# Kernel tuning notes

Measured on AMD Instinct MI355X. Metric: run time of the kernel, lower is better.

The kernel has to match this reference:

```python
import jax, jax.numpy as jnp
import numpy as np

THRESHOLD = 0.5
NEG_POS_RATIO = 3
ALPHA = 10.0


def cxcy_to_xy(c):
    return jnp.concatenate([c[..., :2] - c[..., 2:] / 2, c[..., :2] + c[..., 2:] / 2], axis=-1)


def xy_to_cxcy(xy):
    return jnp.concatenate([(xy[..., :2] + xy[..., 2:]) / 2, xy[..., 2:] - xy[..., :2]], axis=-1)


def encode(cxcy, anc):
    # SSD encoding with variances 0.1 / 0.2 expressed as /10 and *5
    return jnp.concatenate([
        (cxcy[..., :2] - anc[..., :2]) / (anc[..., 2:] / 10.0),
        jnp.log(cxcy[..., 2:] / anc[..., 2:]) * 5.0,
    ], axis=-1)


def jaccard(a, b):
    # a: [N,4] corner boxes, b: [P,4] corner boxes -> [N,P] IoU
    lt = jnp.maximum(a[:, None, :2], b[None, :, :2])
    rb = jnp.minimum(a[:, None, 2:], b[None, :, 2:])
    wh = jnp.clip(rb - lt, 0.0)
    inter = wh[..., 0] * wh[..., 1]
    area_a = (a[:, 2] - a[:, 0]) * (a[:, 3] - a[:, 1])
    area_b = (b[:, 2] - b[:, 0]) * (b[:, 3] - b[:, 1])
    return inter / (area_a[:, None] + area_b[None, :] - inter)


def _match(boxes, labels, corner_anchor, center_anchor):
    # boxes: [N_obj,4] corner, labels: [N_obj]
    n_obj = boxes.shape[0]
    iou = jaccard(boxes, corner_anchor)                 # [N_obj, P]
    obj_idx = jnp.argmax(iou, axis=1)                   # best prior per object
    iou = iou.at[jnp.arange(n_obj), obj_idx].set(1.0)   # force-match best prior
    positive = jnp.any(iou >= THRESHOLD, axis=0)        # [P]
    max_prior_idx = jnp.argmax(iou, axis=0)             # best object per prior
    true_cls = (labels[max_prior_idx] + 1) * positive.astype(jnp.int32)
    true_locs = encode(xy_to_cxcy(boxes[max_prior_idx]), center_anchor)
    return positive, true_cls, true_locs


def setup_inputs() -> dict:
    B, P, C, NOBJ = 32, 24564, 21, 24
    keys = jax.random.split(jax.random.key(0), 7)
    pred_cls = jax.random.normal(keys[0], (B, P, C), dtype=jnp.float32)
    pred_loc = jax.random.normal(keys[1], (B, P, 4), dtype=jnp.float32) * 0.1
    cxy = jax.random.uniform(keys[2], (B, NOBJ, 2), minval=0.2, maxval=0.8)
    wh = jax.random.uniform(keys[3], (B, NOBJ, 2), minval=0.05, maxval=0.3)
    gt_boxes = jnp.clip(jnp.concatenate([cxy - wh / 2, cxy + wh / 2], axis=-1), 0.0, 1.0)
    gt_labels = jax.random.randint(keys[4], (B, NOBJ), 0, C - 1, dtype=jnp.int32)
    a_cxy = jax.random.uniform(keys[5], (P, 2), minval=0.0, maxval=1.0)
    a_wh = jax.random.uniform(keys[6], (P, 2), minval=0.05, maxval=0.4)
    center_anchor = jnp.concatenate([a_cxy, a_wh], axis=-1)
    return {"pred_cls": pred_cls, "pred_loc": pred_loc, "gt_boxes": gt_boxes,
            "gt_labels": gt_labels, "center_anchor": center_anchor}


def reference(pred_cls, pred_loc, gt_boxes, gt_labels, center_anchor):
    B, P, C = pred_cls.shape
    corner_anchor = cxcy_to_xy(center_anchor)
    positive, true_cls, true_locs = jax.vmap(_match, in_axes=(0, 0, None, None))(
        gt_boxes, gt_labels, corner_anchor, center_anchor)

    n_pos = positive.sum(axis=1)                        # [B]
    n_pos_total = n_pos.sum().astype(pred_loc.dtype)

    # localization: L1 mean over positive priors (4 coords each)
    pos_f = positive[..., None].astype(pred_loc.dtype)
    loc_loss = (jnp.abs(pred_loc - true_locs) * pos_f).sum() / (n_pos_total * 4.0)

    # per-element cross entropy [B, P]
    logp = jax.nn.log_softmax(pred_cls, axis=-1)
    ce = -jnp.take_along_axis(logp, true_cls[..., None], axis=-1)[..., 0]

    conf_pos = (ce * positive.astype(ce.dtype)).sum()
    ce_neg = jnp.where(positive, 0.0, ce)
    ce_neg_sorted = jnp.sort(ce_neg, axis=1)[:, ::-1]   # descending
    ranks = jnp.arange(P)[None, :]
    hard_mask = (ranks < (NEG_POS_RATIO * n_pos)[:, None]).astype(ce.dtype)
    conf_neg = (ce_neg_sorted * hard_mask).sum()
    conf_loss = (conf_pos + conf_neg) / n_pos_total

    loc_loss = ALPHA * loc_loss
    total_loss = conf_loss + loc_loss
    return total_loss, (conf_loss, loc_loss)
```

## Files before the change

### kernel.cpp

```cpp
#include <hip/hip_runtime.h>
#include <stdint.h>

#define B 32
#define P 24564
#define NCLS 21
#define NOBJ 24
#define THRESH 0.5f
#define NBKT 2048
#define LCAP 6144
#define BKT_BASE 7232

#define OFF_ACC      0
#define OFF_ARRV     24
#define OFF_NPOS     32
#define HDR_WORDS    40
#define OFF_OBJPART  160
#define OFF_HIST     98464
#define OFF_CENEG    360608

typedef unsigned long long u64;
__device__ __forceinline__ u64 umax64(u64 a, u64 b) { return a > b ? a : b; }

__device__ __forceinline__ int ce_bucket(unsigned bits) {
    int bk = (int)(bits >> 17) - BKT_BASE;
    return bk < 0 ? 0 : (bk > 2047 ? 2047 : bk);
}

__global__ __launch_bounds__(256) void k_objmax(
    const float* __restrict__ gt_boxes, const float* __restrict__ anchor,
    char* __restrict__ ws) {
#pragma clang fp contract(off)
    int b = blockIdx.y;
    int j = blockIdx.x;
    int tid = threadIdx.x;
    unsigned* hist = (unsigned*)(ws + OFF_HIST);
    u64* part = (u64*)(ws + OFF_OBJPART);
    if (tid < 128) hist[(b * 16 + j) * 128 + tid] = 0u;
    if (b == 0 && j == 0 && tid < HDR_WORDS) ((unsigned*)ws)[tid] = 0u;
    __shared__ float4 sbox[NOBJ];
    __shared__ u64 sbest[NOBJ];
    if (tid < NOBJ) {
        const float* g = gt_boxes + (size_t)(b * NOBJ + tid) * 4;
        sbox[tid] = make_float4(g[0], g[1], g[2], g[3]);
        sbest[tid] = 0ull;
    }
    __syncthreads();
    u64 best[NOBJ];
#pragma unroll
    for (int n = 0; n < NOBJ; n++) best[n] = 0ull;
    int pend = min(P, (j + 1) * 1536);
    for (int p = j * 1536 + tid; p < pend; p += 256) {
        float4 a = *(const float4*)(anchor + (size_t)p * 4);
        float ax0 = a.x - a.z * 0.5f, ay0 = a.y - a.w * 0.5f;
        float ax1 = a.x + a.z * 0.5f, ay1 = a.y + a.w * 0.5f;
        float area_a = (ax1 - ax0) * (ay1 - ay0);
        unsigned pk = ~(unsigned)p;
#pragma unroll
        for (int n = 0; n < NOBJ; n++) {
            float4 bx = sbox[n];
            float ltx = fmaxf(bx.x, ax0), lty = fmaxf(bx.y, ay0);
            float rbx = fminf(bx.z, ax1), rby = fminf(bx.w, ay1);
            float w = fmaxf(rbx - ltx, 0.f), h = fmaxf(rby - lty, 0.f);
            float inter = w * h;
            float area_o = (bx.z - bx.x) * (bx.w - bx.y);
            float iou = inter / (area_o + area_a - inter);
            u64 key = ((u64)__float_as_uint(iou) << 32) | pk;
            best[n] = umax64(best[n], key);
        }
    }
#pragma unroll
    for (int n = 0; n < NOBJ; n++) {
        u64 v = best[n];
        for (int off = 32; off > 0; off >>= 1) v = umax64(v, __shfl_down(v, off, 64));
        if ((tid & 63) == 0) atomicMax(&sbest[n], v);
    }
    __syncthreads();
    if (tid < NOBJ) part[((size_t)b * NOBJ + tid) * 16 + j] = sbest[tid];
}

__global__ __launch_bounds__(256, 2) void k_mainB(
    const float* __restrict__ pred_cls, const float* __restrict__ pred_loc,
    const float* __restrict__ gt_boxes, const int* __restrict__ gt_labels,
    const float* __restrict__ anchor, char* __restrict__ ws) {
#pragma clang fp contract(off)
    double* acc = (double*)(ws + OFF_ACC);
    int* n_pos = (int*)(ws + OFF_NPOS);
    const u64* objpart = (const u64*)(ws + OFF_OBJPART);
    unsigned* hist = (unsigned*)(ws + OFF_HIST);
    float* ce_neg = (float*)(ws + OFF_CENEG);

    __shared__ float4 sbox[NOBJ];
    __shared__ int slab[NOBJ];
    __shared__ int sobj[NOBJ];
    __shared__ unsigned shist[NBKT];
    __shared__ float swf[8];
    __shared__ int swi[4];
    const int tid = threadIdx.x;
    const int b = blockIdx.x / 24;
    const int j = blockIdx.x % 24;

    for (int i = tid; i < NBKT; i += 256) shist[i] = 0u;
    if (tid < NOBJ) {
        const float* g = gt_boxes + (size_t)(b * NOBJ + tid) * 4;
        sbox[tid] = make_float4(g[0], g[1], g[2], g[3]);
        slab[tid] = gt_labels[b * NOBJ + tid];
        const u64* pp = objpart + ((size_t)b * NOBJ + tid) * 16;
        u64 m = pp[0];
#pragma unroll
        for (int q = 1; q < 16; q++) m = umax64(m, pp[q]);
        sobj[tid] = (int)(~(unsigned)(m & 0xFFFFFFFFull));
    }
    __syncthreads();

    int p0 = j * 1024 + tid * 4;
    float lsum = 0.f, cpos = 0.f;
    int lnp = 0;
    if (p0 < P) {
        float4 xx[21];
        const float4* xp = (const float4*)(pred_cls + ((size_t)b * P + p0) * NCLS);
#pragma unroll
        for (int k = 0; k < 21; k++) xx[k] = xp[k];
        const float* arr = (const float*)xx;
        float4 anc4[4];
#pragma unroll
        for (int r = 0; r < 4; r++) anc4[r] = ((const float4*)anchor)[p0 + r];
        float4 cev;
        float* cevp = (float*)&cev;
#pragma unroll
        for (int r = 0; r < 4; r++) {
            int p = p0 + r;
            float4 a = anc4[r];
            float ax0 = a.x - a.z * 0.5f, ay0 = a.y - a.w * 0.5f;
            float ax1 = a.x + a.z * 0.5f, ay1 = a.y + a.w * 0.5f;
            float area_a = (ax1 - ax0) * (ay1 - ay0);
            float bv = -1.f;
            int bn = 0;
#pragma unroll
            for (int n = 0; n < NOBJ; n++) {
                float4 bx = sbox[n];
                float ltx = fmaxf(bx.x, ax0), lty = fmaxf(bx.y, ay0);
                float rbx = fminf(bx.z, ax1), rby = fminf(bx.w, ay1);
                float w = fmaxf(rbx - ltx, 0.f), h = fmaxf(rby - lty, 0.f);
                float inter = w * h;
                float area_o = (bx.z - bx.x) * (bx.w - bx.y);
                float iou = inter / (area_o + area_a - inter);
                if (p == sobj[n]) iou = 1.0f;
                if (iou > bv) { bv = iou; bn = n; }
            }
            int pos = (bv >= THRESH) ? 1 : 0;
            int cls = pos ? (slab[bn] + 1) : 0;
            const float* x = arr + r * 21;
            float m = x[0];
#pragma unroll
            for (int q = 1; q < NCLS; q++) m = fmaxf(m, x[q]);
            float s = 0.f;
#pragma unroll
            for (int q = 0; q < NCLS; q++) s += __expf(x[q] - m);
            float xc = x[0];
#pragma unroll
            for (int q = 1; q < NCLS; q++) xc = (cls == q) ? x[q] : xc;
            float ce = m + __logf(s) - xc;
            if (pos) {
                lnp++;
                cpos += ce;
                cevp[r] = 0.f;
                float4 bx = sbox[bn];
                float bcx = (bx.x + bx.z) * 0.5f, bcy = (bx.y + bx.w) * 0.5f;
                float bw = bx.z - bx.x, bh = bx.w - bx.y;
                float t0 = (bcx - a.x) / (a.z / 10.0f);
                float t1 = (bcy - a.y) / (a.w / 10.0f);
                float t2 = __logf(bw / a.z) * 5.0f;
                float t3 = __logf(bh / a.w) * 5.0f;
                float4 pl = *(const float4*)(pred_loc + ((size_t)b * P + p) * 4);
                lsum += fabsf(pl.x - t0) + fabsf(pl.y - t1) + fabsf(pl.z - t2) + fabsf(pl.w - t3);
            } else {
                float cen = fmaxf(ce, 0.f);
                cevp[r] = cen;
                atomicAdd(&shist[ce_bucket(__float_as_uint(cen))], 1u);
            }
        }
        *(float4*)(ce_neg + (size_t)b * P + p0) = cev;
    }
    for (int off = 32; off > 0; off >>= 1) {
        lsum += __shfl_down(lsum, off, 64);
        cpos += __shfl_down(cpos, off, 64);
        lnp  += __shfl_down(lnp, off, 64);
    }
    if ((tid & 63) == 0) { swf[tid >> 6] = lsum; swf[4 + (tid >> 6)] = cpos; swi[tid >> 6] = lnp; }
    __syncthreads();
    if (tid == 0) {
        float ls = swf[0] + swf[1] + swf[2] + swf[3];
        float cs = swf[4] + swf[5] + swf[6] + swf[7];
        int np = swi[0] + swi[1] + swi[2] + swi[3];
        if (np) atomicAdd(&n_pos[b], np);
        atomicAdd(&acc[0], (double)ls);
        atomicAdd(&acc[1], (double)cs);
    }
    for (int i = tid; i < NBKT; i += 256) {
        unsigned c = shist[i];
        if (c) atomicAdd(&hist[b * NBKT + i], c);
    }
}

__device__ __forceinline__ void find_bound(const unsigned* shist, int NB, int K,
                                           int* sscal, unsigned* wsum, int tid) {
    int G = NB >> 8;
    unsigned loc[8];
    unsigned tot = 0;
    for (int g = 0; g < G; g++) { loc[g] = shist[tid * G + g]; tot += loc[g]; }
    unsigned v = tot;
    int lane = tid & 63;
    for (int off = 1; off < 64; off <<= 1) {
        unsigned o = __shfl_down(v, off, 64);
        if (lane + off < 64) v += o;
    }
    if (lane == 0) wsum[tid >> 6] = v;
    __syncthreads();
    unsigned above = 0;
    for (int w = (tid >> 6) + 1; w < 4; w++) above += wsum[w];
    unsigned sfx_excl = above + (v - tot);
    unsigned snext = 0, sloc = 0;
    for (int k = G - 1; k >= 0; k--) {
        sloc = snext + loc[k];
        unsigned sfx_i = sloc + sfx_excl;
        unsigned sfx_n = snext + sfx_excl;
        if (sfx_i >= (unsigned)K && sfx_n < (unsigned)K) {
            sscal[0] = tid * G + k;
            sscal[1] = K - (int)sfx_n;
        }
        snext = sloc;
    }
    if (tid == 0) {
        unsigned total = sloc + sfx_excl;
        if (total < (unsigned)K) {
            sscal[0] = 0;
            sscal[1] = K - (int)((sloc - loc[0]) + sfx_excl);
        }
    }
    __syncthreads();
}

__device__ __forceinline__ void find_bound64(const unsigned* h64, int K, int* sscal, int tid) {
    if (tid < 64) {
        unsigned cnt = h64[tid];
        unsigned v = cnt;
        for (int off = 1; off < 64; off <<= 1) {
            unsigned o = __shfl_down(v, off, 64);
            if (tid + off < 64) v += o;
        }
        unsigned vnext = v - cnt;
        if (v >= (unsigned)K && vnext < (unsigned)K) { sscal[0] = tid; sscal[1] = K - (int)vnext; }
    }
    __syncthreads();
}

__global__ __launch_bounds__(256) void k_sel(
    const float* __restrict__ ce_neg, const unsigned* __restrict__ hist,
    const int* __restrict__ n_pos, double* __restrict__ acc,
    unsigned* __restrict__ arrv, float* __restrict__ out) {
    __shared__ unsigned shist[NBKT];
    __shared__ unsigned slist[LCAP];
    __shared__ int swi[4];
    __shared__ double swd[4];
    __shared__ unsigned wsum[4];
    __shared__ int sscal[4];
    const int b = blockIdx.x;
    const int tid = threadIdx.x;
    const int lane = tid & 63;
    int K = n_pos[b] * 3;
    if (K > P) K = P;
    double s = 0.0;
    if (K > 0) {
        for (int i = tid; i < NBKT; i += 256) shist[i] = hist[b * NBKT + i];
        __syncthreads();
        find_bound(shist, NBKT, K, sscal, wsum, tid);
        int b0 = sscal[0], Kp0 = sscal[1];
        if (tid == 0) sscal[2] = 0;
        __syncthreads();
        const uint4* x4 = (const uint4*)(ce_neg + (size_t)b * P);
        for (int i = tid; i < P / 4; i += 256) {
            uint4 v = x4[i];
            unsigned vv[4] = {v.x, v.y, v.z, v.w};
#pragma unroll
            for (int r = 0; r < 4; r++) {
                int bk = ce_bucket(vv[r]);
                if (bk > b0) s += (double)__uint_as_float(vv[r]);
                else if (bk == b0) {
                    int pos = atomicAdd(&sscal[2], 1);
                    if (pos < LCAP) slist[pos] = vv[r];
                }
            }
        }
        __syncthreads();
        int lcnt = sscal[2];
        if (Kp0 > 0) {
            bool clamped = (b0 == 0) || (b0 == 2047);
            if (lcnt <= LCAP && !clamped) {
                for (int i = tid; i < NBKT; i += 256) shist[i] = 0u;
                __syncthreads();
                for (int i = tid; i < lcnt; i += 256)
                    atomicAdd(&shist[(slist[i] >> 6) & 0x7FFu], 1u);
                __syncthreads();
                find_bound(shist, NBKT, Kp0, sscal, wsum, tid);
                int b1 = sscal[0], Kp1 = sscal[1];
                if (tid < 64) shist[tid] = 0u;
                __syncthreads();
                for (int i = tid; i < lcnt; i += 256) {
                    unsigned v = slist[i];
                    int k1 = (int)((v >> 6) & 0x7FFu);
                    if (k1 > b1) s += (double)__uint_as_float(v);
                    else if (k1 == b1) atomicAdd(&shist[v & 0x3Fu], 1u);
                }
                __syncthreads();
                find_bound64(shist, Kp1, sscal, tid);
                int b2 = sscal[0], R = sscal[1];
                for (int i = tid; i < lcnt; i += 256) {
                    unsigned v = slist[i];
                    if ((int)((v >> 6) & 0x7FFu) == b1 && (int)(v & 0x3Fu) > b2)
                        s += (double)__uint_as_float(v);
                }
                unsigned Tbits = ((unsigned)(b0 + BKT_BASE) << 17) | ((unsigned)b1 << 6) | (unsigned)b2;
                if (tid == 0) s += (double)R * (double)__uint_as_float(Tbits);
            } else if (lcnt <= LCAP) {
                unsigned T = 0;
                for (int bit = 30; bit >= 0; bit--) {
                    unsigned cand = T | (1u << bit);
                    int cc = 0;
                    for (int i = tid; i < lcnt; i += 256) cc += (slist[i] >= cand) ? 1 : 0;
                    for (int off = 32; off > 0; off >>= 1) cc += __shfl_down(cc, off, 64);
                    if (lane == 0) swi[tid >> 6] = cc;
                    __syncthreads();
                    int tot = swi[0] + swi[1] + swi[2] + swi[3];
                    __syncthreads();
                    if (tot >= Kp0) T = cand;
                }
                int cgt = 0;
                for (int i = tid; i < lcnt; i += 256) {
                    unsigned v = slist[i];
                    if (v > T) { cgt++; s += (double)__uint_as_float(v); }
                }
                for (int off = 32; off > 0; off >>= 1) cgt += __shfl_down(cgt, off, 64);
                if (lane == 0) swi[tid >> 6] = cgt;
                __syncthreads();
                if (tid == 0) {
                    int cg = swi[0] + swi[1] + swi[2] + swi[3];
                    s += (double)(Kp0 - cg) * (double)__uint_as_float(T);
                }
                __syncthreads();
            } else {
                const unsigned* src = (const unsigned*)(ce_neg + (size_t)b * P);
                unsigned T = 0;
                for (int bit = 30; bit >= 0; bit--) {
                    unsigned cand = T | (1u << bit);
                    int cc = 0;
                    for (int i = tid; i < P; i += 256) {
                        unsigned v = src[i];
                        if (ce_bucket(v) == b0 && v >= cand) cc++;
                    }
                    for (int off = 32; off > 0; off >>= 1) cc += __shfl_down(cc, off, 64);
                    if (lane == 0) swi[tid >> 6] = cc;
                    __syncthreads();
                    int tot = swi[0] + swi[1] + swi[2] + swi[3];
                    __syncthreads();
                    if (tot >= Kp0) T = cand;
                }
                int cgt = 0;
                for (int i = tid; i < P; i += 256) {
                    unsigned v = src[i];
                    if (ce_bucket(v) == b0 && v > T) { cgt++; s += (double)__uint_as_float(v); }
                }
                for (int off = 32; off > 0; off >>= 1) cgt += __shfl_down(cgt, off, 64);
                if (lane == 0) swi[tid >> 6] = cgt;
                __syncthreads();
                if (tid == 0) {
                    int cg = swi[0] + swi[1] + swi[2] + swi[3];
                    s += (double)(Kp0 - cg) * (double)__uint_as_float(T);
                }
                __syncthreads();
            }
        }
        for (int off = 32; off > 0; off >>= 1) s += __shfl_down(s, off, 64);
        if (lane == 0) swd[tid >> 6] = s;
        __syncthreads();
        if (tid == 0) atomicAdd(&acc[2], swd[0] + swd[1] + swd[2] + swd[3]);
    }
    __syncthreads();
    if (tid == 0) {
        __threadfence();
        unsigned done = __hip_atomic_fetch_add(arrv, 1u, __ATOMIC_ACQ_REL,
                                               __HIP_MEMORY_SCOPE_AGENT);
        if (done == B - 1) {
            int npt = 0;
            for (int k = 0; k < B; k++)
                npt += __hip_atomic_load((int*)&n_pos[k], __ATOMIC_RELAXED,
                                         __HIP_MEMORY_SCOPE_AGENT);
            u64 u0 = __hip_atomic_load((u64*)&acc[0], __ATOMIC_RELAXED, __HIP_MEMORY_SCOPE_AGENT);
            u64 u1 = __hip_atomic_load((u64*)&acc[1], __ATOMIC_RELAXED, __HIP_MEMORY_SCOPE_AGENT);
            u64 u2 = __hip_atomic_load((u64*)&acc[2], __ATOMIC_RELAXED, __HIP_MEMORY_SCOPE_AGENT);
            double a0 = __longlong_as_double((long long)u0);
            double a1 = __longlong_as_double((long long)u1);
            double a2 = __longlong_as_double((long long)u2);
            double npf = (double)npt;
            float conf = (float)((a1 + a2) / npf);
            float loc = 10.0f * (float)(a0 / (npf * 4.0));
            out[0] = conf + loc;
            out[1] = conf;
            out[2] = loc;
        }
    }
}

extern "C" void kernel_launch(void* const* d_in, const int* in_sizes, int n_in,
                              void* d_out, int out_size, void* d_ws, size_t ws_size,
                              hipStream_t stream) {
    const float* pred_cls = (const float*)d_in[0];
    const float* pred_loc = (const float*)d_in[1];
    const float* gt_boxes = (const float*)d_in[2];
    const int*   gt_labels = (const int*)d_in[3];
    const float* anchor   = (const float*)d_in[4];
    float* out = (float*)d_out;
    char* ws = (char*)d_ws;
    double* acc = (double*)(ws + OFF_ACC);
    unsigned* arrv = (unsigned*)(ws + OFF_ARRV);
    int* n_pos = (int*)(ws + OFF_NPOS);
    unsigned* hist = (unsigned*)(ws + OFF_HIST);
    float* ce_neg = (float*)(ws + OFF_CENEG);

    k_objmax<<<dim3(16, B), 256, 0, stream>>>(gt_boxes, anchor, ws);
    k_mainB<<<24 * B, 256, 0, stream>>>(pred_cls, pred_loc, gt_boxes, gt_labels, anchor, ws);
    k_sel<<<B, 256, 0, stream>>>(ce_neg, hist, n_pos, acc, arrv, out);
}
```

Before: 180.2 us.

## Fuse hard-negative selection into main kernel via last-block-per-batch arrival

Merges the per-batch hard-negative selection kernel into the main loss kernel. Each block bumps a per-batch arrival counter, and the 24th block to finish a batch runs the histogram bound search and top-K sum for that batch. A global counter still finalizes the output. This removes one kernel launch and lets selection for early batches overlap with main work on other batches. In exchange it raises shared memory per block with the selection list, which may pressure occupancy, and relies on atomics and fences for cross-block visibility.

```diff
diff --git a/kernel.cpp b/kernel.cpp
--- a/kernel.cpp
+++ b/kernel.cpp
@@ -11,12 +11,13 @@
 #define BKT_BASE 7232
 
 #define OFF_ACC      0
-#define OFF_ARRV     24
-#define OFF_NPOS     32
-#define HDR_WORDS    40
-#define OFF_OBJPART  160
-#define OFF_HIST     98464
-#define OFF_CENEG    360608
+#define OFF_ARRVALL  24
+#define OFF_BARRV    32
+#define OFF_NPOS     160
+#define HDR_WORDS    72
+#define OFF_OBJPART  288
+#define OFF_HIST     98592
+#define OFF_CENEG    360736
 
 typedef unsigned long long u64;
 __device__ __forceinline__ u64 umax64(u64 a, u64 b) { return a > b ? a : b; }
@@ -78,12 +79,66 @@
     if (tid < NOBJ) part[((size_t)b * NOBJ + tid) * 16 + j] = sbest[tid];
 }
 
-__global__ __launch_bounds__(256, 2) void k_mainB(
+__device__ __forceinline__ void find_bound(const unsigned* shist, int NB, int K,
+                                           int* sscal, unsigned* wsum, int tid) {
+    int G = NB >> 8;
+    unsigned loc[8];
+    unsigned tot = 0;
+    for (int g = 0; g < G; g++) { loc[g] = shist[tid * G + g]; tot += loc[g]; }
+    unsigned v = tot;
+    int lane = tid & 63;
+    for (int off = 1; off < 64; off <<= 1) {
+        unsigned o = __shfl_down(v, off, 64);
+        if (lane + off < 64) v += o;
+    }
+    if (lane == 0) wsum[tid >> 6] = v;
+    __syncthreads();
+    unsigned above = 0;
+    for (int w = (tid >> 6) + 1; w < 4; w++) above += wsum[w];
+    unsigned sfx_excl = above + (v - tot);
+    unsigned snext = 0, sloc = 0;
+    for (int k = G - 1; k >= 0; k--) {
+        sloc = snext + loc[k];
+        unsigned sfx_i = sloc + sfx_excl;
+        unsigned sfx_n = snext + sfx_excl;
+        if (sfx_i >= (unsigned)K && sfx_n < (unsigned)K) {
+            sscal[0] = tid * G + k;
+            sscal[1] = K - (int)sfx_n;
+        }
+        snext = sloc;
+    }
+    if (tid == 0) {
+        unsigned total = sloc + sfx_excl;
+        if (total < (unsigned)K) {
+            sscal[0] = 0;
+            sscal[1] = K - (int)((sloc - loc[0]) + sfx_excl);
+        }
+    }
+    __syncthreads();
+}
+
+__device__ __forceinline__ void find_bound64(const unsigned* h64, int K, int* sscal, int tid) {
+    if (tid < 64) {
+        unsigned cnt = h64[tid];
+        unsigned v = cnt;
+        for (int off = 1; off < 64; off <<= 1) {
+            unsigned o = __shfl_down(v, off, 64);
+            if (tid + off < 64) v += o;
+        }
+        unsigned vnext = v - cnt;
+        if (v >= (unsigned)K && vnext < (unsigned)K) { sscal[0] = tid; sscal[1] = K - (int)vnext; }
+    }
+    __syncthreads();
+}
+
+__global__ __launch_bounds__(256, 2) void k_fused(
     const float* __restrict__ pred_cls, const float* __restrict__ pred_loc,
     const float* __restrict__ gt_boxes, const int* __restrict__ gt_labels,
-    const float* __restrict__ anchor, char* __restrict__ ws) {
+    const float* __restrict__ anchor, char* __restrict__ ws, float* __restrict__ out) {
 #pragma clang fp contract(off)
     double* acc = (double*)(ws + OFF_ACC);
+    unsigned* arrv_all = (unsigned*)(ws + OFF_ARRVALL);
+    unsigned* batch_arrv = (unsigned*)(ws + OFF_BARRV);
     int* n_pos = (int*)(ws + OFF_NPOS);
     const u64* objpart = (const u64*)(ws + OFF_OBJPART);
     unsigned* hist = (unsigned*)(ws + OFF_HIST);
@@ -93,9 +148,16 @@
     __shared__ int slab[NOBJ];
     __shared__ int sobj[NOBJ];
     __shared__ unsigned shist[NBKT];
+    __shared__ unsigned slist[LCAP];
     __shared__ float swf[8];
     __shared__ int swi[4];
+    __shared__ double swd[4];
+    __shared__ unsigned wsum[4];
+    __shared__ int sscal[4];
+    __shared__ int swin;
+
     const int tid = threadIdx.x;
+    const int lane = tid & 63;
     const int b = blockIdx.x / 24;
     const int j = blockIdx.x % 24;
 
@@ -186,7 +248,7 @@
         cpos += __shfl_down(cpos, off, 64);
         lnp  += __shfl_down(lnp, off, 64);
     }
-    if ((tid & 63) == 0) { swf[tid >> 6] = lsum; swf[4 + (tid >> 6)] = cpos; swi[tid >> 6] = lnp; }
+    if (lane == 0) { swf[tid >> 6] = lsum; swf[4 + (tid >> 6)] = cpos; swi[tid >> 6] = lnp; }
     __syncthreads();
     if (tid == 0) {
         float ls = swf[0] + swf[1] + swf[2] + swf[3];
@@ -200,78 +262,25 @@
         unsigned c = shist[i];
         if (c) atomicAdd(&hist[b * NBKT + i], c);
     }
-}
-
-__device__ __forceinline__ void find_bound(const unsigned* shist, int NB, int K,
-                                           int* sscal, unsigned* wsum, int tid) {
-    int G = NB >> 8;
-    unsigned loc[8];
-    unsigned tot = 0;
-    for (int g = 0; g < G; g++) { loc[g] = shist[tid * G + g]; tot += loc[g]; }
-    unsigned v = tot;
-    int lane = tid & 63;
-    for (int off = 1; off < 64; off <<= 1) {
-        unsigned o = __shfl_down(v, off, 64);
-        if (lane + off < 64) v += o;
-    }
-    if (lane == 0) wsum[tid >> 6] = v;
-    __syncthreads();
-    unsigned above = 0;
-    for (int w = (tid >> 6) + 1; w < 4; w++) above += wsum[w];
-    unsigned sfx_excl = above + (v - tot);
-    unsigned snext = 0, sloc = 0;
-    for (int k = G - 1; k >= 0; k--) {
-        sloc = snext + loc[k];
-        unsigned sfx_i = sloc + sfx_excl;
-        unsigned sfx_n = snext + sfx_excl;
-        if (sfx_i >= (unsigned)K && sfx_n < (unsigned)K) {
-            sscal[0] = tid * G + k;
-            sscal[1] = K - (int)sfx_n;
-        }
-        snext = sloc;
-    }
+
+    __syncthreads();
     if (tid == 0) {
-        unsigned total = sloc + sfx_excl;
-        if (total < (unsigned)K) {
-            sscal[0] = 0;
-            sscal[1] = K - (int)((sloc - loc[0]) + sfx_excl);
-        }
-    }
-    __syncthreads();
-}
-
-__device__ __forceinline__ void find_bound64(const unsigned* h64, int K, int* sscal, int tid) {
-    if (tid < 64) {
-        unsigned cnt = h64[tid];
-        unsigned v = cnt;
-        for (int off = 1; off < 64; off <<= 1) {
-            unsigned o = __shfl_down(v, off, 64);
-            if (tid + off < 64) v += o;
-        }
-        unsigned vnext = v - cnt;
-        if (v >= (unsigned)K && vnext < (unsigned)K) { sscal[0] = tid; sscal[1] = K - (int)vnext; }
-    }
-    __syncthreads();
-}
-
-__global__ __launch_bounds__(256) void k_sel(
-    const float* __restrict__ ce_neg, const unsigned* __restrict__ hist,
-    const int* __restrict__ n_pos, double* __restrict__ acc,
-    unsigned* __restrict__ arrv, float* __restrict__ out) {
-    __shared__ unsigned shist[NBKT];
-    __shared__ unsigned slist[LCAP];
-    __shared__ int swi[4];
-    __shared__ double swd[4];
-    __shared__ unsigned wsum[4];
-    __shared__ int sscal[4];
-    const int b = blockIdx.x;
-    const int tid = threadIdx.x;
-    const int lane = tid & 63;
-    int K = n_pos[b] * 3;
+        __threadfence();
+        unsigned old = __hip_atomic_fetch_add(&batch_arrv[b], 1u,
+                                              __ATOMIC_ACQ_REL, __HIP_MEMORY_SCOPE_AGENT);
+        swin = (old == 23) ? 1 : 0;
+    }
+    __syncthreads();
+    if (swin == 0) return;
+
+    int npb = __hip_atomic_load(&n_pos[b], __ATOMIC_RELAXED, __HIP_MEMORY_SCOPE_AGENT);
+    int K = npb * 3;
     if (K > P) K = P;
     double s = 0.0;
     if (K > 0) {
-        for (int i = tid; i < NBKT; i += 256) shist[i] = hist[b * NBKT + i];
+        for (int i = tid; i < NBKT; i += 256)
+            shist[i] = __hip_atomic_load(&hist[b * NBKT + i],
+                                         __ATOMIC_RELAXED, __HIP_MEMORY_SCOPE_AGENT);
         __syncthreads();
         find_bound(shist, NBKT, K, sscal, wsum, tid);
         int b0 = sscal[0], Kp0 = sscal[1];
@@ -384,16 +393,16 @@
         __syncthreads();
         if (tid == 0) atomicAdd(&acc[2], swd[0] + swd[1] + swd[2] + swd[3]);
     }
+
     __syncthreads();
     if (tid == 0) {
         __threadfence();
-        unsigned done = __hip_atomic_fetch_add(arrv, 1u, __ATOMIC_ACQ_REL,
-                                               __HIP_MEMORY_SCOPE_AGENT);
-        if (done == B - 1) {
+        unsigned old = __hip_atomic_fetch_add(arrv_all, 1u,
+                                              __ATOMIC_ACQ_REL, __HIP_MEMORY_SCOPE_AGENT);
+        if (old == B - 1) {
             int npt = 0;
             for (int k = 0; k < B; k++)
-                npt += __hip_atomic_load((int*)&n_pos[k], __ATOMIC_RELAXED,
-                                         __HIP_MEMORY_SCOPE_AGENT);
+                npt += __hip_atomic_load(&n_pos[k], __ATOMIC_RELAXED, __HIP_MEMORY_SCOPE_AGENT);
             u64 u0 = __hip_atomic_load((u64*)&acc[0], __ATOMIC_RELAXED, __HIP_MEMORY_SCOPE_AGENT);
             u64 u1 = __hip_atomic_load((u64*)&acc[1], __ATOMIC_RELAXED, __HIP_MEMORY_SCOPE_AGENT);
             u64 u2 = __hip_atomic_load((u64*)&acc[2], __ATOMIC_RELAXED, __HIP_MEMORY_SCOPE_AGENT);
@@ -420,13 +429,8 @@
     const float* anchor   = (const float*)d_in[4];
     float* out = (float*)d_out;
     char* ws = (char*)d_ws;
-    double* acc = (double*)(ws + OFF_ACC);
-    unsigned* arrv = (unsigned*)(ws + OFF_ARRV);
-    int* n_pos = (int*)(ws + OFF_NPOS);
-    unsigned* hist = (unsigned*)(ws + OFF_HIST);
-    float* ce_neg = (float*)(ws + OFF_CENEG);
 
     k_objmax<<<dim3(16, B), 256, 0, stream>>>(gt_boxes, anchor, ws);
-    k_mainB<<<24 * B, 256, 0, stream>>>(pred_cls, pred_loc, gt_boxes, gt_labels, anchor, ws);
-    k_sel<<<B, 256, 0, stream>>>(ce_neg, hist, n_pos, acc, arrv, out);
-}
+    k_fused<<<24 * B, 256, 0, stream>>>(pred_cls, pred_loc, gt_boxes, gt_labels,
+                                        anchor, ws, out);
+}
```

Result: slower. 213.4 us (+18.4%).

## Halve per-thread work in main kernel and widen selection kernel to 1024 threads

Applied to the files above, without the earlier changes.

The main kernel now gives each thread 2 priors instead of 4. That doubles the grid to 48 blocks per image and raises the launch-bounds occupancy hint from 2 to 4, to get more waves in flight and fewer registers per thread. The IoU loop now reads precomputed box areas from shared memory and uses a hardware reciprocal instead of a divide, with fp contraction re-enabled. The selection kernel runs with 1024 threads per block, with a 16-wave block reduction helper and find_bound restricted to the first 256 threads. In exchange it accepts small numeric differences from the approximate reciprocal and FMA contraction, plus more per-block histogram flush atomics.

```diff
diff --git a/kernel.cpp b/kernel.cpp
--- a/kernel.cpp
+++ b/kernel.cpp
@@ -78,11 +78,10 @@
     if (tid < NOBJ) part[((size_t)b * NOBJ + tid) * 16 + j] = sbest[tid];
 }
 
-__global__ __launch_bounds__(256, 2) void k_mainB(
+__global__ __launch_bounds__(256, 4) void k_mainB(
     const float* __restrict__ pred_cls, const float* __restrict__ pred_loc,
     const float* __restrict__ gt_boxes, const int* __restrict__ gt_labels,
     const float* __restrict__ anchor, char* __restrict__ ws) {
-#pragma clang fp contract(off)
     double* acc = (double*)(ws + OFF_ACC);
     int* n_pos = (int*)(ws + OFF_NPOS);
     const u64* objpart = (const u64*)(ws + OFF_OBJPART);
@@ -90,19 +89,21 @@
     float* ce_neg = (float*)(ws + OFF_CENEG);
 
     __shared__ float4 sbox[NOBJ];
+    __shared__ float sarea[NOBJ];
     __shared__ int slab[NOBJ];
     __shared__ int sobj[NOBJ];
     __shared__ unsigned shist[NBKT];
     __shared__ float swf[8];
     __shared__ int swi[4];
     const int tid = threadIdx.x;
-    const int b = blockIdx.x / 24;
-    const int j = blockIdx.x % 24;
+    const int b = blockIdx.x / 48;
+    const int j = blockIdx.x % 48;
 
     for (int i = tid; i < NBKT; i += 256) shist[i] = 0u;
     if (tid < NOBJ) {
         const float* g = gt_boxes + (size_t)(b * NOBJ + tid) * 4;
         sbox[tid] = make_float4(g[0], g[1], g[2], g[3]);
+        sarea[tid] = (g[2] - g[0]) * (g[3] - g[1]);
         slab[tid] = gt_labels[b * NOBJ + tid];
         const u64* pp = objpart + ((size_t)b * NOBJ + tid) * 16;
         u64 m = pp[0];
@@ -112,24 +113,24 @@
     }
     __syncthreads();
 
-    int p0 = j * 1024 + tid * 4;
+    int p0 = j * 512 + tid * 2;
     float lsum = 0.f, cpos = 0.f;
     int lnp = 0;
     if (p0 < P) {
-        float4 xx[21];
-        const float4* xp = (const float4*)(pred_cls + ((size_t)b * P + p0) * NCLS);
+        float2 xx[21];
+        const float2* xp = (const float2*)(pred_cls + ((size_t)b * P + p0) * NCLS);
 #pragma unroll
         for (int k = 0; k < 21; k++) xx[k] = xp[k];
         const float* arr = (const float*)xx;
-        float4 anc4[4];
-#pragma unroll
-        for (int r = 0; r < 4; r++) anc4[r] = ((const float4*)anchor)[p0 + r];
-        float4 cev;
+        float4 anc2[2];
+        anc2[0] = ((const float4*)anchor)[p0];
+        anc2[1] = ((const float4*)anchor)[p0 + 1];
+        float2 cev;
         float* cevp = (float*)&cev;
 #pragma unroll
-        for (int r = 0; r < 4; r++) {
+        for (int r = 0; r < 2; r++) {
             int p = p0 + r;
-            float4 a = anc4[r];
+            float4 a = anc2[r];
             float ax0 = a.x - a.z * 0.5f, ay0 = a.y - a.w * 0.5f;
             float ax1 = a.x + a.z * 0.5f, ay1 = a.y + a.w * 0.5f;
             float area_a = (ax1 - ax0) * (ay1 - ay0);
@@ -142,8 +143,8 @@
                 float rbx = fminf(bx.z, ax1), rby = fminf(bx.w, ay1);
                 float w = fmaxf(rbx - ltx, 0.f), h = fmaxf(rby - lty, 0.f);
                 float inter = w * h;
-                float area_o = (bx.z - bx.x) * (bx.w - bx.y);
-                float iou = inter / (area_o + area_a - inter);
+                float den = sarea[n] + area_a - inter;
+                float iou = inter * __builtin_amdgcn_rcpf(den);
                 if (p == sobj[n]) iou = 1.0f;
                 if (iou > bv) { bv = iou; bn = n; }
             }
@@ -179,7 +180,7 @@
                 atomicAdd(&shist[ce_bucket(__float_as_uint(cen))], 1u);
             }
         }
-        *(float4*)(ce_neg + (size_t)b * P + p0) = cev;
+        *(float2*)(ce_neg + (size_t)b * P + p0) = cev;
     }
     for (int off = 32; off > 0; off >>= 1) {
         lsum += __shfl_down(lsum, off, 64);
@@ -206,35 +207,39 @@
                                            int* sscal, unsigned* wsum, int tid) {
     int G = NB >> 8;
     unsigned loc[8];
-    unsigned tot = 0;
-    for (int g = 0; g < G; g++) { loc[g] = shist[tid * G + g]; tot += loc[g]; }
-    unsigned v = tot;
-    int lane = tid & 63;
-    for (int off = 1; off < 64; off <<= 1) {
-        unsigned o = __shfl_down(v, off, 64);
-        if (lane + off < 64) v += o;
-    }
-    if (lane == 0) wsum[tid >> 6] = v;
-    __syncthreads();
-    unsigned above = 0;
-    for (int w = (tid >> 6) + 1; w < 4; w++) above += wsum[w];
-    unsigned sfx_excl = above + (v - tot);
-    unsigned snext = 0, sloc = 0;
-    for (int k = G - 1; k >= 0; k--) {
-        sloc = snext + loc[k];
-        unsigned sfx_i = sloc + sfx_excl;
-        unsigned sfx_n = snext + sfx_excl;
-        if (sfx_i >= (unsigned)K && sfx_n < (unsigned)K) {
-            sscal[0] = tid * G + k;
-            sscal[1] = K - (int)sfx_n;
-        }
-        snext = sloc;
-    }
-    if (tid == 0) {
-        unsigned total = sloc + sfx_excl;
-        if (total < (unsigned)K) {
-            sscal[0] = 0;
-            sscal[1] = K - (int)((sloc - loc[0]) + sfx_excl);
+    unsigned tot = 0, v = 0;
+    if (tid < 256) {
+        for (int g = 0; g < G; g++) { loc[g] = shist[tid * G + g]; tot += loc[g]; }
+        v = tot;
+        int lane = tid & 63;
+        for (int off = 1; off < 64; off <<= 1) {
+            unsigned o = __shfl_down(v, off, 64);
+            if (lane + off < 64) v += o;
+        }
+        if (lane == 0) wsum[tid >> 6] = v;
+    }
+    __syncthreads();
+    if (tid < 256) {
+        unsigned above = 0;
+        for (int w = (tid >> 6) + 1; w < 4; w++) above += wsum[w];
+        unsigned sfx_excl = above + (v - tot);
+        unsigned snext = 0, sloc = 0;
+        for (int k = G - 1; k >= 0; k--) {
+            sloc = snext + loc[k];
+            unsigned sfx_i = sloc + sfx_excl;
+            unsigned sfx_n = snext + sfx_excl;
+            if (sfx_i >= (unsigned)K && sfx_n < (unsigned)K) {
+                sscal[0] = tid * G + k;
+                sscal[1] = K - (int)sfx_n;
+            }
+            snext = sloc;
+        }
+        if (tid == 0) {
+            unsigned total = sloc + sfx_excl;
+            if (total < (unsigned)K) {
+                sscal[0] = 0;
+                sscal[1] = K - (int)((sloc - loc[0]) + sfx_excl);
+            }
         }
     }
     __syncthreads();
@@ -254,31 +259,41 @@
     __syncthreads();
 }
 
-__global__ __launch_bounds__(256) void k_sel(
+__device__ __forceinline__ int bsum16i(int v, int* buf, int tid) {
+    for (int off = 32; off > 0; off >>= 1) v += __shfl_down(v, off, 64);
+    if ((tid & 63) == 0) buf[tid >> 6] = v;
+    __syncthreads();
+    int r = 0;
+#pragma unroll
+    for (int w = 0; w < 16; w++) r += buf[w];
+    __syncthreads();
+    return r;
+}
+
+__global__ __launch_bounds__(1024) void k_sel(
     const float* __restrict__ ce_neg, const unsigned* __restrict__ hist,
     const int* __restrict__ n_pos, double* __restrict__ acc,
     unsigned* __restrict__ arrv, float* __restrict__ out) {
     __shared__ unsigned shist[NBKT];
     __shared__ unsigned slist[LCAP];
-    __shared__ int swi[4];
-    __shared__ double swd[4];
+    __shared__ int swi[16];
+    __shared__ double swd[16];
     __shared__ unsigned wsum[4];
     __shared__ int sscal[4];
     const int b = blockIdx.x;
     const int tid = threadIdx.x;
-    const int lane = tid & 63;
     int K = n_pos[b] * 3;
     if (K > P) K = P;
     double s = 0.0;
     if (K > 0) {
-        for (int i = tid; i < NBKT; i += 256) shist[i] = hist[b * NBKT + i];
+        for (int i = tid; i < NBKT; i += 1024) shist[i] = hist[b * NBKT + i];
         __syncthreads();
         find_bound(shist, NBKT, K, sscal, wsum, tid);
         int b0 = sscal[0], Kp0 = sscal[1];
         if (tid == 0) sscal[2] = 0;
         __syncthreads();
         const uint4* x4 = (const uint4*)(ce_neg + (size_t)b * P);
-        for (int i = tid; i < P / 4; i += 256) {
+        for (int i = tid; i < P / 4; i += 1024) {
             uint4 v = x4[i];
             unsigned vv[4] = {v.x, v.y, v.z, v.w};
 #pragma unroll
@@ -296,16 +311,16 @@
         if (Kp0 > 0) {
             bool clamped = (b0 == 0) || (b0 == 2047);
             if (lcnt <= LCAP && !clamped) {
-                for (int i = tid; i < NBKT; i += 256) shist[i] = 0u;
+                for (int i = tid; i < NBKT; i += 1024) shist[i] = 0u;
                 __syncthreads();
-                for (int i = tid; i < lcnt; i += 256)
+                for (int i = tid; i < lcnt; i += 1024)
                     atomicAdd(&shist[(slist[i] >> 6) & 0x7FFu], 1u);
                 __syncthreads();
                 find_bound(shist, NBKT, Kp0, sscal, wsum, tid);
                 int b1 = sscal[0], Kp1 = sscal[1];
                 if (tid < 64) shist[tid] = 0u;
                 __syncthreads();
-                for (int i = tid; i < lcnt; i += 256) {
+                for (int i = tid; i < lcnt; i += 1024) {
                     unsigned v = slist[i];
                     int k1 = (int)((v >> 6) & 0x7FFu);
                     if (k1 > b1) s += (double)__uint_as_float(v);
@@ -314,7 +329,7 @@
                 __syncthreads();
                 find_bound64(shist, Kp1, sscal, tid);
                 int b2 = sscal[0], R = sscal[1];
-                for (int i = tid; i < lcnt; i += 256) {
+                for (int i = tid; i < lcnt; i += 1024) {
                     unsigned v = slist[i];
                     if ((int)((v >> 6) & 0x7FFu) == b1 && (int)(v & 0x3Fu) > b2)
                         s += (double)__uint_as_float(v);
@@ -326,63 +341,48 @@
                 for (int bit = 30; bit >= 0; bit--) {
                     unsigned cand = T | (1u << bit);
                     int cc = 0;
-                    for (int i = tid; i < lcnt; i += 256) cc += (slist[i] >= cand) ? 1 : 0;
-                    for (int off = 32; off > 0; off >>= 1) cc += __shfl_down(cc, off, 64);
-                    if (lane == 0) swi[tid >> 6] = cc;
-                    __syncthreads();
-                    int tot = swi[0] + swi[1] + swi[2] + swi[3];
-                    __syncthreads();
+                    for (int i = tid; i < lcnt; i += 1024) cc += (slist[i] >= cand) ? 1 : 0;
+                    int tot = bsum16i(cc, swi, tid);
                     if (tot >= Kp0) T = cand;
                 }
                 int cgt = 0;
-                for (int i = tid; i < lcnt; i += 256) {
+                for (int i = tid; i < lcnt; i += 1024) {
                     unsigned v = slist[i];
                     if (v > T) { cgt++; s += (double)__uint_as_float(v); }
                 }
-                for (int off = 32; off > 0; off >>= 1) cgt += __shfl_down(cgt, off, 64);
-                if (lane == 0) swi[tid >> 6] = cgt;
-                __syncthreads();
-                if (tid == 0) {
-                    int cg = swi[0] + swi[1] + swi[2] + swi[3];
-                    s += (double)(Kp0 - cg) * (double)__uint_as_float(T);
-                }
-                __syncthreads();
+                int cg = bsum16i(cgt, swi, tid);
+                if (tid == 0) s += (double)(Kp0 - cg) * (double)__uint_as_float(T);
             } else {
                 const unsigned* src = (const unsigned*)(ce_neg + (size_t)b * P);
                 unsigned T = 0;
                 for (int bit = 30; bit >= 0; bit--) {
                     unsigned cand = T | (1u << bit);
                     int cc = 0;
-                    for (int i = tid; i < P; i += 256) {
+                    for (int i = tid; i < P; i += 1024) {
                         unsigned v = src[i];
                         if (ce_bucket(v) == b0 && v >= cand) cc++;
                     }
-                    for (int off = 32; off > 0; off >>= 1) cc += __shfl_down(cc, off, 64);
-                    if (lane == 0) swi[tid >> 6] = cc;
-                    __syncthreads();
-                    int tot = swi[0] + swi[1] + swi[2] + swi[3];
-                    __syncthreads();
+                    int tot = bsum16i(cc, swi, tid);
                     if (tot >= Kp0) T = cand;
                 }
                 int cgt = 0;
-                for (int i = tid; i < P; i += 256) {
+                for (int i = tid; i < P; i += 1024) {
                     unsigned v = src[i];
                     if (ce_bucket(v) == b0 && v > T) { cgt++; s += (double)__uint_as_float(v); }
                 }
-                for (int off = 32; off > 0; off >>= 1) cgt += __shfl_down(cgt, off, 64);
-                if (lane == 0) swi[tid >> 6] = cgt;
-                __syncthreads();
-                if (tid == 0) {
-                    int cg = swi[0] + swi[1] + swi[2] + swi[3];
-                    s += (double)(Kp0 - cg) * (double)__uint_as_float(T);
-                }
-                __syncthreads();
+                int cg = bsum16i(cgt, swi, tid);
+                if (tid == 0) s += (double)(Kp0 - cg) * (double)__uint_as_float(T);
             }
         }
         for (int off = 32; off > 0; off >>= 1) s += __shfl_down(s, off, 64);
-        if (lane == 0) swd[tid >> 6] = s;
+        if ((tid & 63) == 0) swd[tid >> 6] = s;
         __syncthreads();
-        if (tid == 0) atomicAdd(&acc[2], swd[0] + swd[1] + swd[2] + swd[3]);
+        if (tid == 0) {
+            double tot = 0.0;
+#pragma unroll
+            for (int w = 0; w < 16; w++) tot += swd[w];
+            atomicAdd(&acc[2], tot);
+        }
     }
     __syncthreads();
     if (tid == 0) {
@@ -427,6 +427,6 @@
     float* ce_neg = (float*)(ws + OFF_CENEG);
 
     k_objmax<<<dim3(16, B), 256, 0, stream>>>(gt_boxes, anchor, ws);
-    k_mainB<<<24 * B, 256, 0, stream>>>(pred_cls, pred_loc, gt_boxes, gt_labels, anchor, ws);
-    k_sel<<<B, 256, 0, stream>>>(ce_neg, hist, n_pos, acc, arrv, out);
-}
+    k_mainB<<<48 * B, 256, 0, stream>>>(pred_cls, pred_loc, gt_boxes, gt_labels, anchor, ws);
+    k_sel<<<B, 1024, 0, stream>>>(ce_neg, hist, n_pos, acc, arrv, out);
+}
```

Measured after the change: 198.0 us. 9.9% more time.
